# Kernel optimization log

Measured on AMD Instinct MI355X. Metric: run time of the kernel, lower is better.

Reference implementation:

```python
import jax, jax.numpy as jnp
import numpy as np

RATIO = 4   # downsample_ratio = 2 * (resolution[0] / swin_res_threshold)
KTOP = 1    # k_top_samples default


def setup_inputs() -> dict:
    key = jax.random.key(0)
    kA, kB, kC, kD, kattn = jax.random.split(key, 5)
    Bt, Cd, H, W, heads = 8, 256, 64, 64, 8
    Nl = (H // RATIO) * (W // RATIO)  # 256
    return {
        "A": jax.random.normal(kA, (Bt, Cd, H, W), dtype=jnp.float32),
        "B": jax.random.normal(kB, (Bt, Cd, H, W), dtype=jnp.float32),
        "C": jax.random.normal(kC, (Bt, Cd, H, W), dtype=jnp.float32),
        "D": jax.random.normal(kD, (Bt, Cd, H, W), dtype=jnp.float32),
        "attn": jax.random.normal(kattn, (Bt, heads, Nl, Nl), dtype=jnp.float32),
    }


def _guided_resampler(v, coarse, ratio, k):
    # v: [Bt, Cd, H, W]; coarse: [Bt, N_low, N_low]
    Bt, Cd, H, W = v.shape
    Hl, Wl = H // ratio, W // ratio
    Nh, Nl = H * W, Hl * Wl
    r2 = ratio * ratio

    v_seq = v.reshape(Bt, Cd, Nh).transpose(0, 2, 1)          # [Bt, Nh, Cd]

    topv, topi = jax.lax.top_k(coarse, k)                     # [Bt, Nl, k]
    tl_row = (topi // Wl) * ratio                             # top-left of r x r window
    tl_col = (topi % Wl) * ratio
    dr, dc = jnp.meshgrid(jnp.arange(ratio), jnp.arange(ratio), indexing="ij")
    rows = tl_row[..., None] + dr.reshape(-1)                 # [Bt, Nl, k, r2]
    cols = tl_col[..., None] + dc.reshape(-1)
    sparse_1d = (rows * W + cols).reshape(Bt, Nl, k * r2)     # [Bt, Nl, k*r2]

    q = jnp.arange(Nh)
    low_idx = (q // W) // ratio * Wl + (q % W) // ratio       # [Nh] high->low cell map

    final_idx = sparse_1d[:, low_idx, :]                      # [Bt, Nh, k*r2]
    v_sparse = v_seq[jnp.arange(Bt)[:, None, None], final_idx]  # [Bt, Nh, k*r2, Cd]

    w_low = jax.nn.softmax(topv, axis=-1)                     # [Bt, Nl, k]
    w_high = w_low[:, low_idx, :]                             # [Bt, Nh, k]

    v_r = v_sparse.reshape(Bt, Nh, k, r2, Cd)
    w_b = (w_high / r2)[..., None, None]                      # [Bt, Nh, k, 1, 1]
    warped = (v_r * w_b).sum(axis=(2, 3))                     # [Bt, Nh, Cd]
    return warped.transpose(0, 2, 1).reshape(Bt, Cd, H, W)


def reference(A, B, C, D, attn):
    # Fine stage (resolution >= swin_res_threshold): only C and attn are used.
    coarse = attn.mean(axis=1)  # [Bt, N_low, N_low]
    return _guided_resampler(C, coarse, RATIO, KTOP)
```

## Files before the change

### kernel.cpp

```cpp
#include <hip/hip_runtime.h>
#include <hip/hip_bf16.h>


__global__ void ca_argmax_kernel(const float* __restrict__ attn,
                                 int* __restrict__ best) {
    int bl = blockIdx.x;
    int b  = bl >> 8;
    int l  = bl & 255;
    int j  = threadIdx.x;

    const float* base = attn + (((size_t)b * 8) * 256 + l) * 256;
    float s = 0.0f;
#pragma unroll
    for (int h = 0; h < 8; ++h)
        s += base[(size_t)h * 256 * 256 + j];

    __shared__ float sval[256];
    __shared__ int   sidx[256];
    sval[j] = s;
    sidx[j] = j;
    __syncthreads();
#pragma unroll
    for (int off = 128; off > 0; off >>= 1) {
        if (j < off) {
            float v2 = sval[j + off];
            int   i2 = sidx[j + off];
            if (v2 > sval[j] || (v2 == sval[j] && i2 < sidx[j])) {
                sval[j] = v2;
                sidx[j] = i2;
            }
        }
        __syncthreads();
    }
    if (j == 0) best[bl] = sidx[0];
}

__global__ void ca_resample_kernel(const float* __restrict__ C,
                                   const int* __restrict__ best,
                                   float* __restrict__ out) {
    int bc = blockIdx.x;
    int b  = bc >> 8;
    int t  = threadIdx.x;

    __shared__ __align__(16) float plane[64 * 64];
    __shared__ float cellavg[256];

    const float4* src4   = reinterpret_cast<const float4*>(C + (size_t)bc * 4096);
    float4*       plane4 = reinterpret_cast<float4*>(plane);
#pragma unroll
    for (int i = 0; i < 4; ++i)
        plane4[t + i * 256] = src4[t + i * 256];
    __syncthreads();

    {
        int jstar = best[b * 256 + t];
        int tr = (jstar >> 4) << 2;
        int tc = (jstar & 15) << 2;
        float s = 0.0f;
#pragma unroll
        for (int r = 0; r < 4; ++r) {
            float4 v = *reinterpret_cast<const float4*>(&plane[(tr + r) * 64 + tc]);
            s += (v.x + v.y) + (v.z + v.w);
        }
        cellavg[t] = s * (1.0f / 16.0f);
    }
    __syncthreads();

    float4* out4 = reinterpret_cast<float4*>(out + (size_t)bc * 4096);
#pragma unroll
    for (int i = 0; i < 4; ++i) {
        int q4  = i * 1024 + t * 4;
        int row = q4 >> 6;
        int col = q4 & 63;
        float v = cellavg[(row >> 2) * 16 + (col >> 2)];
        out4[t + i * 256] = make_float4(v, v, v, v);
    }
}

extern "C" void kernel_launch(void* const* d_in, const int* in_sizes, int n_in,
                              void* d_out, int out_size, void* d_ws, size_t ws_size,
                              hipStream_t stream) {
    const float* C    = (const float*)d_in[2];
    const float* attn = (const float*)d_in[4];
    float* out = (float*)d_out;
    int* best  = (int*)d_ws;

    ca_argmax_kernel<<<2048, 256, 0, stream>>>(attn, best);
    ca_resample_kernel<<<2048, 256, 0, stream>>>(C, best, out);
}
```

Before: 21.01 us.

## Fuse argmax and resample into one cooperative kernel with grid sync

Merges the attention argmax and the resample into a single cooperative kernel that loads each C plane into registers, computes per-cell means while the attention sum is reduced, then uses a grid-wide sync before gathering the selected cell means. It also changes the fallback resample kernel to precompute all cell means instead of staging the full plane in shared memory. The aim is to drop one kernel launch and overlap C loads with the argmax. The cost is a grid barrier, per-call host occupancy and attribute queries, and the requirement that all 2048 blocks be co-resident.

```diff
diff --git a/kernel.cpp b/kernel.cpp
--- a/kernel.cpp
+++ b/kernel.cpp
@@ -1,6 +1,74 @@
 #include <hip/hip_runtime.h>
 #include <hip/hip_bf16.h>
+#include <hip/hip_cooperative_groups.h>
 
+namespace cg = cooperative_groups;
+
+__global__ __launch_bounds__(256, 8) void ca_fused_kernel(
+    const float* __restrict__ C,
+    const float* __restrict__ attn,
+    int* __restrict__ best,
+    float* __restrict__ out)
+{
+    int bi = blockIdx.x;
+    int b  = bi >> 8;
+    int t  = threadIdx.x;
+
+    __shared__ float bmean[256];
+    __shared__ float sval[256];
+    __shared__ int   sidx[256];
+
+    const float* pbase = C + (size_t)bi * 4096 + ((t >> 4) * 4) * 64 + (t & 15) * 4;
+    float4 r0 = *reinterpret_cast<const float4*>(pbase);
+    float4 r1 = *reinterpret_cast<const float4*>(pbase + 64);
+    float4 r2 = *reinterpret_cast<const float4*>(pbase + 128);
+    float4 r3 = *reinterpret_cast<const float4*>(pbase + 192);
+
+    const float* abase = attn + (((size_t)b * 8) * 256 + (bi & 255)) * 256;
+    float s = 0.0f;
+#pragma unroll
+    for (int h = 0; h < 8; ++h)
+        s += abase[(size_t)h * 65536 + t];
+
+    bmean[t] = ((r0.x + r0.y) + (r0.z + r0.w) + (r1.x + r1.y) + (r1.z + r1.w) +
+                (r2.x + r2.y) + (r2.z + r2.w) + (r3.x + r3.y) + (r3.z + r3.w)) *
+               (1.0f / 16.0f);
+
+    sval[t] = s;
+    sidx[t] = t;
+    __syncthreads();
+#pragma unroll
+    for (int off = 128; off > 0; off >>= 1) {
+        if (t < off) {
+            float v2 = sval[t + off];
+            int   i2 = sidx[t + off];
+            if (v2 > sval[t] || (v2 == sval[t] && i2 < sidx[t])) {
+                sval[t] = v2;
+                sidx[t] = i2;
+            }
+        }
+        __syncthreads();
+    }
+    if (t == 0) best[bi] = sidx[0];
+
+    cg::this_grid().sync();
+
+    int   jstar = best[b * 256 + t];
+    float v     = bmean[jstar];
+    __syncthreads();
+    sval[t] = v;
+    __syncthreads();
+
+    float4* out4 = reinterpret_cast<float4*>(out + (size_t)bi * 4096);
+#pragma unroll
+    for (int i = 0; i < 4; ++i) {
+        int q4  = i * 1024 + t * 4;
+        int row = q4 >> 6;
+        int col = q4 & 63;
+        float w = sval[(row >> 2) * 16 + (col >> 2)];
+        out4[t + i * 256] = make_float4(w, w, w, w);
+    }
+}
 
 __global__ void ca_argmax_kernel(const float* __restrict__ attn,
                                  int* __restrict__ best) {
@@ -13,7 +81,7 @@
     float s = 0.0f;
 #pragma unroll
     for (int h = 0; h < 8; ++h)
-        s += base[(size_t)h * 256 * 256 + j];
+        s += base[(size_t)h * 65536 + j];
 
     __shared__ float sval[256];
     __shared__ int   sidx[256];
@@ -42,28 +110,20 @@
     int b  = bc >> 8;
     int t  = threadIdx.x;
 
-    __shared__ __align__(16) float plane[64 * 64];
+    __shared__ float bmean[256];
     __shared__ float cellavg[256];
 
-    const float4* src4   = reinterpret_cast<const float4*>(C + (size_t)bc * 4096);
-    float4*       plane4 = reinterpret_cast<float4*>(plane);
-#pragma unroll
-    for (int i = 0; i < 4; ++i)
-        plane4[t + i * 256] = src4[t + i * 256];
+    const float* pbase = C + (size_t)bc * 4096 + ((t >> 4) * 4) * 64 + (t & 15) * 4;
+    float4 r0 = *reinterpret_cast<const float4*>(pbase);
+    float4 r1 = *reinterpret_cast<const float4*>(pbase + 64);
+    float4 r2 = *reinterpret_cast<const float4*>(pbase + 128);
+    float4 r3 = *reinterpret_cast<const float4*>(pbase + 192);
+    bmean[t] = ((r0.x + r0.y) + (r0.z + r0.w) + (r1.x + r1.y) + (r1.z + r1.w) +
+                (r2.x + r2.y) + (r2.z + r2.w) + (r3.x + r3.y) + (r3.z + r3.w)) *
+               (1.0f / 16.0f);
     __syncthreads();
 
-    {
-        int jstar = best[b * 256 + t];
-        int tr = (jstar >> 4) << 2;
-        int tc = (jstar & 15) << 2;
-        float s = 0.0f;
-#pragma unroll
-        for (int r = 0; r < 4; ++r) {
-            float4 v = *reinterpret_cast<const float4*>(&plane[(tr + r) * 64 + tc]);
-            s += (v.x + v.y) + (v.z + v.w);
-        }
-        cellavg[t] = s * (1.0f / 16.0f);
-    }
+    cellavg[t] = bmean[best[b * 256 + t]];
     __syncthreads();
 
     float4* out4 = reinterpret_cast<float4*>(out + (size_t)bc * 4096);
@@ -85,6 +145,22 @@
     float* out = (float*)d_out;
     int* best  = (int*)d_ws;
 
-    ca_argmax_kernel<<<2048, 256, 0, stream>>>(attn, best);
-    ca_resample_kernel<<<2048, 256, 0, stream>>>(C, best, out);
+    int coop = 0, ncu = 0, blocksPerCU = 0;
+    hipDeviceGetAttribute(&coop, hipDeviceAttributeCooperativeLaunch, 0);
+    hipDeviceGetAttribute(&ncu, hipDeviceAttributeMultiprocessorCount, 0);
+    hipOccupancyMaxActiveBlocksPerMultiprocessor(
+        &blocksPerCU, reinterpret_cast<const void*>(ca_fused_kernel), 256, 0);
+
+    bool coop_ok = false;
+    if (coop && (long)blocksPerCU * ncu >= 2048) {
+        void* args[] = { (void*)&C, (void*)&attn, (void*)&best, (void*)&out };
+        hipError_t e = hipLaunchCooperativeKernel(
+            reinterpret_cast<void*>(ca_fused_kernel),
+            dim3(2048), dim3(256), args, 0, stream);
+        coop_ok = (e == hipSuccess);
+    }
+    if (!coop_ok) {
+        ca_argmax_kernel<<<2048, 256, 0, stream>>>(attn, best);
+        ca_resample_kernel<<<2048, 256, 0, stream>>>(C, best, out);
+    }
 }
```

Result: no change. 20.68 us (-1.6%).
